# Performance work log

Hardware: AMD Instinct MI355X
Metric: run time of the kernel (lower is better)

Reference implementation:

```python
import jax, jax.numpy as jnp
import numpy as np
from jax import lax

ALPHA = 0.7

def _ema(x, alpha):
    # x: [B, L, C]; sequential EMA along L via lax.scan
    x0 = x[:, 0, :]                       # [B, C]
    xs = jnp.moveaxis(x[:, 1:, :], 1, 0)  # [L-1, B, C]
    def step(carry, xt):
        new = alpha * xt + (1.0 - alpha) * carry
        return new, new
    _, ys = lax.scan(step, x0, xs)        # ys: [L-1, B, C]
    return jnp.concatenate([x0[:, None, :], jnp.moveaxis(ys, 0, 1)], axis=1)


def setup_inputs() -> dict:
    key = jax.random.key(0)
    k1, k2 = jax.random.split(key)
    B, L, C = 32, 4096, 512
    x = jax.random.normal(k1, (B, L, C), dtype=jnp.float32)
    gate = jnp.float32(0.5)  # learnable scalar gate parameter (gate_init)
    return {"x": x, "gate": gate}


def reference(x, gate):
    # trend computed under torch.no_grad -> constant w.r.t. autodiff
    trend = lax.stop_gradient(_ema(x, ALPHA))
    seasonal = x - trend
    g = jnp.clip(gate, 0.0, 1.0)
    return g * seasonal + (1.0 - g) * trend
```

## Files before the change

kernel.cpp:

```cpp
#include <hip/hip_runtime.h>


constexpr int B   = 32;
constexpr int L   = 4096;
constexpr int C   = 512;
constexpr int CV  = C / 4;
constexpr int CH  = 64;
constexpr int NCH = L / CH;
constexpr int H   = 12;
constexpr float ALPHA = 0.7f;

typedef float f32x4 __attribute__((ext_vector_type(4)));

__device__ __forceinline__ void nt_store4(float4* p, const float4& v) {
    f32x4 w = {v.x, v.y, v.z, v.w};
    __builtin_nontemporal_store(w, reinterpret_cast<f32x4*>(p));
}

__device__ __forceinline__ float4 ema_step(float4 t, float4 xv, float a, float na) {
    float4 r;
    r.x = fmaf(a, xv.x, na * t.x);
    r.y = fmaf(a, xv.y, na * t.y);
    r.z = fmaf(a, xv.z, na * t.z);
    r.w = fmaf(a, xv.w, na * t.w);
    return r;
}

__global__ __launch_bounds__(256, 4) void STAR_47605417509306_kernel(
        const float4* __restrict__ x, const float* __restrict__ gate,
        float4* __restrict__ out) {
    const int tid   = blockIdx.x * blockDim.x + threadIdx.x;
    const int c4    = tid & (CV - 1);
    const int rest  = tid / CV;
    const int chunk = rest & (NCH - 1);
    const int b     = rest / NCH;

    float g = gate[0];
    g = fminf(fmaxf(g, 0.0f), 1.0f);
    const float a  = ALPHA;
    const float na = 1.0f - ALPHA;
    const float c2 = 1.0f - 2.0f * g;

    const int base = (b * L) * CV + c4;
    const int l0   = chunk * CH;

    float4 t;
    int lstart;
    if (chunk == 0) {
        t = x[base];
        float4 o;
        o.x = fmaf(g, t.x, c2 * t.x);
        o.y = fmaf(g, t.y, c2 * t.y);
        o.z = fmaf(g, t.z, c2 * t.z);
        o.w = fmaf(g, t.w, c2 * t.w);
        nt_store4(&out[base], o);
        lstart = 1;
    } else {
        t = x[base + (l0 - H) * CV];
#pragma unroll
        for (int l = l0 - H + 1; l < l0; ++l) {
            float4 xv = x[base + l * CV];
            t = ema_step(t, xv, a, na);
        }
        lstart = l0;
    }

#pragma unroll 8
    for (int l = lstart; l < l0 + CH; ++l) {
        float4 xv = x[base + l * CV];
        t = ema_step(t, xv, a, na);
        float4 o;
        o.x = fmaf(g, xv.x, c2 * t.x);
        o.y = fmaf(g, xv.y, c2 * t.y);
        o.z = fmaf(g, xv.z, c2 * t.z);
        o.w = fmaf(g, xv.w, c2 * t.w);
        nt_store4(&out[base + l * CV], o);
    }
}

extern "C" void kernel_launch(void* const* d_in, const int* in_sizes, int n_in,
                              void* d_out, int out_size, void* d_ws, size_t ws_size,
                              hipStream_t stream) {
    const float4* x    = (const float4*)d_in[0];
    const float*  gate = (const float*)d_in[1];
    float4* out        = (float4*)d_out;

    const int total_threads = B * NCH * CV;
    const int block = 256;
    const int grid  = total_threads / block;
    STAR_47605417509306_kernel<<<grid, block, 0, stream>>>(x, gate, out);
}
```

Baseline: 451.9 us.

## Double chunk length and software-pipeline loads with explicit scheduling barriers

Doubles the chunk length so each thread handles 128 timesteps, which halves the redundant 12-step warm-up reads. The main loop becomes a four-buffer rotation that prefetches two batches of four rows ahead, with sched_barrier keeping loads, compute and stores in separate phases. The warm-up loads are also issued all at once before the recurrence runs. In exchange, launch bounds drop to two blocks per SIMD and the thread count halves, which costs occupancy and latency hiding on a memory-bound kernel.

```diff
diff --git a/kernel.cpp b/kernel.cpp
--- a/kernel.cpp
+++ b/kernel.cpp
@@ -5,9 +5,11 @@
 constexpr int L   = 4096;
 constexpr int C   = 512;
 constexpr int CV  = C / 4;
-constexpr int CH  = 64;
+constexpr int CH  = 128;
 constexpr int NCH = L / CH;
 constexpr int H   = 12;
+constexpr int BT  = 4;
+constexpr int NB  = CH / BT;
 constexpr float ALPHA = 0.7f;
 
 typedef float f32x4 __attribute__((ext_vector_type(4)));
@@ -26,7 +28,7 @@
     return r;
 }
 
-__global__ __launch_bounds__(256, 4) void STAR_47605417509306_kernel(
+__global__ __launch_bounds__(256, 2) void STAR_47605417509306_kernel(
         const float4* __restrict__ x, const float* __restrict__ gate,
         float4* __restrict__ out) {
     const int tid   = blockIdx.x * blockDim.x + threadIdx.x;
@@ -45,37 +47,71 @@
     const int l0   = chunk * CH;
 
     float4 t;
-    int lstart;
     if (chunk == 0) {
         t = x[base];
-        float4 o;
-        o.x = fmaf(g, t.x, c2 * t.x);
-        o.y = fmaf(g, t.y, c2 * t.y);
-        o.z = fmaf(g, t.z, c2 * t.z);
-        o.w = fmaf(g, t.w, c2 * t.w);
-        nt_store4(&out[base], o);
-        lstart = 1;
     } else {
-        t = x[base + (l0 - H) * CV];
+        float4 h[H];
 #pragma unroll
-        for (int l = l0 - H + 1; l < l0; ++l) {
-            float4 xv = x[base + l * CV];
-            t = ema_step(t, xv, a, na);
-        }
-        lstart = l0;
+        for (int i = 0; i < H; ++i) h[i] = x[base + (l0 - H + i) * CV];
+        t = h[0];
+#pragma unroll
+        for (int i = 1; i < H; ++i) t = ema_step(t, h[i], a, na);
     }
 
-#pragma unroll 8
-    for (int l = lstart; l < l0 + CH; ++l) {
-        float4 xv = x[base + l * CV];
-        t = ema_step(t, xv, a, na);
-        float4 o;
-        o.x = fmaf(g, xv.x, c2 * t.x);
-        o.y = fmaf(g, xv.y, c2 * t.y);
-        o.z = fmaf(g, xv.z, c2 * t.z);
-        o.w = fmaf(g, xv.w, c2 * t.w);
-        nt_store4(&out[base + l * CV], o);
+    float4 X0[BT], X1[BT], X2[BT], X3[BT];
+
+#define LOADB(Xj, k)                                                   \
+    do {                                                               \
+        _Pragma("unroll")                                              \
+        for (int i = 0; i < BT; ++i)                                   \
+            Xj[i] = x[base + (l0 + (k) * BT + i) * CV];                \
+    } while (0)
+
+#define COMPB(Xj)                                                      \
+    do {                                                               \
+        _Pragma("unroll")                                              \
+        for (int i = 0; i < BT; ++i) {                                 \
+            t = ema_step(t, Xj[i], a, na);                             \
+            float4 o;                                                  \
+            o.x = fmaf(g, Xj[i].x, c2 * t.x);                          \
+            o.y = fmaf(g, Xj[i].y, c2 * t.y);                          \
+            o.z = fmaf(g, Xj[i].z, c2 * t.z);                          \
+            o.w = fmaf(g, Xj[i].w, c2 * t.w);                          \
+            Xj[i] = o;                                                 \
+        }                                                              \
+    } while (0)
+
+#define STORB(Xj, k)                                                   \
+    do {                                                               \
+        _Pragma("unroll")                                              \
+        for (int i = 0; i < BT; ++i)                                   \
+            nt_store4(&out[base + (l0 + (k) * BT + i) * CV], Xj[i]);   \
+    } while (0)
+
+#define BODY(k, Xcur, Xpre)                                            \
+    do {                                                               \
+        if ((k) + 2 < NB) LOADB(Xpre, (k) + 2);                        \
+        __builtin_amdgcn_sched_barrier(0);                             \
+        COMPB(Xcur);                                                   \
+        __builtin_amdgcn_sched_barrier(0);                             \
+        STORB(Xcur, (k));                                              \
+        __builtin_amdgcn_sched_barrier(0);                             \
+    } while (0)
+
+    LOADB(X0, 0);
+    LOADB(X1, 1);
+
+    for (int kk = 0; kk < NB; kk += 4) {
+        BODY(kk + 0, X0, X2);
+        BODY(kk + 1, X1, X3);
+        BODY(kk + 2, X2, X0);
+        BODY(kk + 3, X3, X1);
     }
+
+#undef LOADB
+#undef COMPB
+#undef STORB
+#undef BODY
 }
 
 extern "C" void kernel_launch(void* const* d_in, const int* in_sizes, int n_in,
```

New measurement: 451.7 us. Within noise of the previous version (-0.1%).
